# Performance work log

Measured on AMD Instinct MI355X. Metric: run time of the kernel, lower is better.

The kernel has to match this reference:

```python
import jax, jax.numpy as jnp
import numpy as np

N_NODES = 20000
N_EDGES = 8192
UNITS = 128
NUM_GAUSSIANS = 50
CUTOFF = 8.0
GAMMA = 10.0
MIN_DIST, MAX_DIST = 0.0, 30.0


def setup_inputs() -> dict:
    key = jax.random.key(0)
    ks = jax.random.split(key, 6)
    node_features = jax.random.normal(ks[0], (N_NODES, UNITS), dtype=jnp.float32)
    edge_indices = jax.random.randint(ks[1], (2, N_EDGES), 0, N_NODES, dtype=jnp.int32)
    distances = jax.random.uniform(ks[2], (N_EDGES,), dtype=jnp.float32)
    # filter network params (Dense(units) -> swish -> Dense(units*units))
    W1 = jax.random.normal(ks[3], (NUM_GAUSSIANS, UNITS), dtype=jnp.float32) / np.sqrt(NUM_GAUSSIANS)
    b1 = jnp.zeros((UNITS,), dtype=jnp.float32)
    W2 = jax.random.normal(ks[4], (UNITS, UNITS * UNITS), dtype=jnp.float32) / np.sqrt(UNITS)
    b2 = jnp.zeros((UNITS * UNITS,), dtype=jnp.float32)
    # transform Dense(units, use_bias=False)
    Wt = jax.random.normal(ks[5], (UNITS, UNITS), dtype=jnp.float32) / np.sqrt(UNITS)
    return {"node_features": node_features, "edge_indices": edge_indices,
            "distances": distances, "W1": W1, "b1": b1, "W2": W2, "b2": b2, "Wt": Wt}


def reference(node_features, edge_indices, distances, W1, b1, W2, b2, Wt):
    n_nodes, units = node_features.shape
    # cutoff mask (multiplicative; dropped edges contribute zero to the scatter-sum,
    # equivalent to tf.boolean_mask + unsorted_segment_sum)
    mask = (distances <= CUTOFF).astype(node_features.dtype)  # [E]
    # Gaussian basis expansion
    centers = jnp.linspace(MIN_DIST, MAX_DIST, NUM_GAUSSIANS, dtype=jnp.float32)
    df = jnp.exp(-GAMMA * jnp.square(distances[:, None] - centers[None, :]))  # [E, G]
    # filter network: Dense -> swish -> Dense(units*units)
    h = jax.nn.silu(df @ W1 + b1)                    # [E, U]
    filters = (h @ W2 + b2).reshape(-1, units, units)  # [E, U, U]
    # gather source node features, transform, per-edge matvec
    src = node_features[edge_indices[0]]             # [E, U]
    transformed = src @ Wt                           # [E, U]
    filtered = jnp.einsum('eij,ej->ei', filters, transformed) * mask[:, None]  # [E, U]
    # scatter-sum to destination nodes
    messages = jax.ops.segment_sum(filtered, edge_indices[1], num_segments=n_nodes)
    return jax.nn.silu(messages)
```

## Files before the change

### kernel.cpp

```cpp
#include <hip/hip_runtime.h>
#include <hip/hip_fp16.h>


typedef _Float16 f16;
typedef __attribute__((ext_vector_type(8))) f16 f16x8;
typedef __attribute__((ext_vector_type(4))) float f32x4;
typedef __attribute__((ext_vector_type(4))) unsigned int u32x4;

#define NEDGE 8192
#define NNODE 20000
#define NG    50
#define KSTEPS 516
#define W2C_BYTES (KSTEPS * 8192)
#define HT_BYTES (64 * 132 * 128 * 2)
#define TM_BYTES (NEDGE * 128 * 2)
#define WTC_BYTES (4 * 8 * 64 * 8 * 2)
#define W1C_BYTES (2 * 8 * 64 * 8 * 2)
#define FP_BYTES ((size_t)8 * NEDGE * 128 * 4)

#define LDS_H   0
#define LDS_TM  5120
#define LDS_TOT 37888

#define K1_SRC 0
#define K1_DF  16384
#define K1_MSK 24576
#define K1_TOT 24832

static __device__ __forceinline__ float fsilu(float x) { return x / (1.0f + __expf(-x)); }

static __device__ __forceinline__ void gll16(const void* g, void* l) {
  __builtin_amdgcn_global_load_lds(
      (const __attribute__((address_space(1))) unsigned int*)g,
      (__attribute__((address_space(3))) unsigned int*)l, 16, 0, 0);
}

__global__ __launch_bounds__(256) void kprep(const float* __restrict__ W2,
                                             const float* __restrict__ b2,
                                             const float* __restrict__ W1,
                                             const float* __restrict__ B1,
                                             const float* __restrict__ WT,
                                             f16* __restrict__ w2c,
                                             f16* __restrict__ wtc,
                                             f16* __restrict__ w1c,
                                             float* __restrict__ out, int nz4) {
  const int bid = blockIdx.x, tid = threadIdx.x;

  if (bid < 516) {
    const int u = bid >> 2, s = bid & 3;
    const int i = tid >> 1, half = tid & 1;
    const float* src = ((u < 128) ? (W2 + (size_t)u * 16384) : b2)
                       + i * 128 + s * 32 + half * 16;
    union { f16 s16[16]; u32x4 v[2]; } pk;
#pragma unroll
    for (int q = 0; q < 4; ++q) {
      f32x4 v = *(const f32x4*)(src + q * 4);
#pragma unroll
      for (int r = 0; r < 4; ++r) pk.s16[q * 4 + r] = (f16)v[r];
    }
    const int nt = i >> 4, l15 = i & 15;
    u32x4* dst = (u32x4*)w2c + (size_t)(u * 4 + s) * 512 + nt * 64 + l15;
    dst[(half * 2 + 0) * 16] = pk.v[0];
    dst[(half * 2 + 1) * 16] = pk.v[1];
    return;
  }
  if (bid < 520) {
    int step = bid - 516;
#pragma unroll
    for (int q = 0; q < 2; ++q) {
      int fi = q * 256 + tid;
      int lane = fi & 63, nt = fi >> 6;
      int j = nt * 16 + (lane & 15);
      union { f16 s[8]; u32x4 v; } pk;
#pragma unroll
      for (int r = 0; r < 8; ++r) {
        int u = step * 32 + (lane >> 4) * 8 + r;
        pk.s[r] = (f16)WT[u * 128 + j];
      }
      *((u32x4*)wtc + (step * 8 + nt) * 64 + lane) = pk.v;
    }
    return;
  }
  if (bid == 520) {
#pragma unroll
    for (int q = 0; q < 4; ++q) {
      int fi = q * 256 + tid;
      int lane = fi & 63, nt = (fi >> 6) & 7, step = fi >> 9;
      int j = nt * 16 + (lane & 15);
      union { f16 s[8]; u32x4 v; } pk;
#pragma unroll
      for (int r = 0; r < 8; ++r) {
        int g = step * 32 + (lane >> 4) * 8 + r;
        float v = (g < 50) ? W1[g * 128 + j] : ((g == 63) ? B1[j] : 0.0f);
        pk.s[r] = (f16)v;
      }
      *((u32x4*)w1c + (step * 8 + nt) * 64 + lane) = pk.v;
    }
    return;
  }
  {
    int base = (bid - 521) * 1024;
    f32x4 z = {0.f, 0.f, 0.f, 0.f};
#pragma unroll
    for (int k = 0; k < 4; ++k) {
      int i4 = base + k * 256 + tid;
      if (i4 < nz4) ((f32x4*)out)[i4] = z;
    }
  }
}

__global__ __launch_bounds__(256) void k1m(const float* __restrict__ NF,
                                           const int*   __restrict__ EI,
                                           const float* __restrict__ DI,
                                           const f16* __restrict__ wtc,
                                           const f16* __restrict__ w1c,
                                           f16* __restrict__ ht2,
                                           f16* __restrict__ tmo) {
  __shared__ u32x4 smem_v[K1_TOT / 16];
  char* smem = (char*)smem_v;
  const int bid = blockIdx.x, tid = threadIdx.x;
  const int e0g = bid * 64;
  const int eb  = bid >> 1;
  const int el0 = (bid & 1) * 64;

  if (tid < 64) {
    float d = DI[e0g + tid];
    *(float*)(smem + K1_MSK + tid * 4) = (d <= 8.0f) ? 1.0f : 0.0f;
  }
  {
    int e = tid >> 2, g0 = (tid & 3) * 16;
    float d = DI[e0g + e];
    union { f16 s[16]; u32x4 v[2]; } pk;
#pragma unroll
    for (int gg = 0; gg < 16; ++gg) {
      int g = g0 + gg;
      float x = d - (float)g * (30.0f / 49.0f);
      float v = (g < 50) ? __expf(-10.0f * x * x) : ((g == 63) ? 1.0f : 0.0f);
      pk.s[gg] = (f16)v;
    }
    int base = e * 128 + g0 * 2, sw = (e & 7) << 4;
    *(u32x4*)(smem + K1_DF + ((base) ^ sw))      = pk.v[0];
    *(u32x4*)(smem + K1_DF + ((base + 16) ^ sw)) = pk.v[1];
  }
#pragma unroll
  for (int p = 0; p < 8; ++p) {
    int e = p * 8 + (tid >> 5);
    int u0 = (tid & 31) * 4;
    int row = EI[e0g + e];
    f32x4 v = *(const f32x4*)(NF + (size_t)row * 128 + u0);
    union { f16 s[4]; unsigned long long q; } pk;
#pragma unroll
    for (int r = 0; r < 4; ++r) pk.s[r] = (f16)v[r];
    int addr = e * 256 + u0 * 2;
    *(unsigned long long*)(smem + K1_SRC + (addr ^ ((e & 7) << 4))) = pk.q;
  }
  __syncthreads();

  const int w = tid >> 6, lane = tid & 63;
  const int l15 = lane & 15, g4 = lane >> 4;
  const int erow = w * 16;
  const int asw = (l15 & 7) << 4;

  f32x4 at[8], ah[8];
#pragma unroll
  for (int nt = 0; nt < 8; ++nt) {
    at[nt] = (f32x4){0.f, 0.f, 0.f, 0.f};
    ah[nt] = (f32x4){0.f, 0.f, 0.f, 0.f};
  }
  const f16x8* wtp = (const f16x8*)wtc;
  const f16x8* w1p = (const f16x8*)w1c;

#pragma unroll
  for (int step = 0; step < 4; ++step) {
    int aaddr = (erow + l15) * 256 + step * 64 + g4 * 16;
    f16x8 a = *(const f16x8*)(smem + K1_SRC + (aaddr ^ asw));
#pragma unroll
    for (int nt = 0; nt < 8; ++nt)
      at[nt] = __builtin_amdgcn_mfma_f32_16x16x32_f16(a, wtp[(step * 8 + nt) * 64 + lane], at[nt], 0, 0, 0);
  }
#pragma unroll
  for (int step = 0; step < 2; ++step) {
    int aaddr = (erow + l15) * 128 + step * 64 + g4 * 16;
    f16x8 a = *(const f16x8*)(smem + K1_DF + (aaddr ^ asw));
#pragma unroll
    for (int nt = 0; nt < 8; ++nt)
      ah[nt] = __builtin_amdgcn_mfma_f32_16x16x32_f16(a, w1p[(step * 8 + nt) * 64 + lane], ah[nt], 0, 0, 0);
  }

  const float* mk = (const float*)(smem + K1_MSK);
#pragma unroll
  for (int r = 0; r < 4; ++r) {
    int el_ = erow + g4 * 4 + r;
    float m = mk[el_];
    int sw2 = (el_ & 7) << 4;
    char* rowp = (char*)tmo + (size_t)(e0g + el_) * 256;
#pragma unroll
    for (int nt = 0; nt < 8; ++nt)
      *(f16*)(rowp + (((nt * 16 + l15) * 2) ^ sw2)) = (f16)(m * at[nt][r]);
  }
#pragma unroll
  for (int r = 0; r < 4; ++r) {
    int el_ = el0 + erow + g4 * 4 + r;
#pragma unroll
    for (int nt = 0; nt < 8; ++nt) {
      int u = nt * 16 + l15;
      ht2[((size_t)eb * 132 + u) * 128 + el_] = (f16)fsilu(ah[nt][r]);
    }
  }
  if (tid < 64) ht2[((size_t)eb * 132 + 128) * 128 + el0 + tid] = (f16)1.0f;
}

template<int MODE>
__global__ __launch_bounds__(256, 2) void k2_gemm(const f16* __restrict__ w2c,
                                                  const f16* __restrict__ ht2,
                                                  const f16* __restrict__ tm,
                                                  const int* __restrict__ EI,
                                                  float* __restrict__ fpart,
                                                  float* __restrict__ msg) {
  __shared__ u32x4 smem_v[LDS_TOT / 16];
  char* smem = (char*)smem_v;

  const int bid = blockIdx.x;
  const int c   = bid & 7;
  const int eb  = bid >> 3;
  const int e0  = eb * 128;
  const int nu  = (c == 7) ? 17 : 16;
  const int tid = threadIdx.x, w = tid >> 6, lane = tid & 63;
  const int l15 = lane & 15, g4 = lane >> 4;
  const int wm = w >> 1, wn = w & 1;

  const char* bp = (const char*)w2c + (size_t)(c * 64) * 8192 + wn * 4096 + lane * 16;
  f16x8 B0[4], B1[4];
#pragma unroll
  for (int nt = 0; nt < 4; ++nt) B0[nt] = *(const f16x8*)(bp + nt * 1024);
#pragma unroll
  for (int nt = 0; nt < 4; ++nt) B1[nt] = *(const f16x8*)(bp + 8192 + nt * 1024);

  {
    const char* tsrc = (const char*)tm + (size_t)e0 * 256 + w * 8192;
#pragma unroll
    for (int q = 0; q < 8; ++q)
      gll16(tsrc + q * 1024 + lane * 16,
            smem + LDS_TM + w * 8192 + q * 1024 + lane * 16);
  }
  if (w == 0) {
    const char* hsrc = (const char*)ht2 + ((size_t)eb * 132 + c * 16) * 256;
#pragma unroll
    for (int q = 0; q < 5; ++q)
      gll16(hsrc + q * 1024 + lane * 16, smem + LDS_H + q * 1024 + lane * 16);
  }
  __syncthreads();

  f16x8 Tall[4][4];
  {
    const int tmrow = LDS_TM + (wm * 64 + l15) * 256;
    const int colsw = (l15 & 7) << 4;
#pragma unroll
    for (int rt = 0; rt < 4; ++rt)
#pragma unroll
      for (int jc = 0; jc < 4; ++jc)
        Tall[rt][jc] = *(const f16x8*)(smem + tmrow + rt * 4096 +
                                       ((jc * 64 + g4 * 16) ^ colsw));
  }
  const __half* hbase = (const __half*)(smem + LDS_H) + wm * 64 + l15;

  __half2 hc[4], hn[4];
#pragma unroll
  for (int rt = 0; rt < 4; ++rt) hc[rt] = __half2half2(hbase[rt * 16]);

  size_t off = 2 * 8192;
  f32x4 acc[4][4];
#pragma unroll
  for (int rt = 0; rt < 4; ++rt)
#pragma unroll
    for (int nt = 0; nt < 4; ++nt) acc[rt][nt] = (f32x4){0.f, 0.f, 0.f, 0.f};

  for (int u = 0; u < nu; ++u) {
#pragma unroll
    for (int jc = 0; jc < 4; ++jc) {
      if (jc == 1) {
#pragma unroll
        for (int rt = 0; rt < 4; ++rt)
          hn[rt] = __half2half2(hbase[(u + 1) * 128 + rt * 16]);
      }
      union uf { f16x8 v; __half2 h[4]; };
      uf a[4];
#pragma unroll
      for (int rt = 0; rt < 4; ++rt) {
        uf t; t.v = Tall[rt][jc];
#pragma unroll
        for (int q = 0; q < 4; ++q) a[rt].h[q] = __hmul2(t.h[q], hc[rt]);
      }
      __builtin_amdgcn_s_setprio(1);
#pragma unroll
      for (int nt = 0; nt < 4; ++nt) {
        if ((jc & 1) == 0) {
#pragma unroll
          for (int rt = 0; rt < 4; ++rt)
            acc[rt][nt] = __builtin_amdgcn_mfma_f32_16x16x32_f16(a[rt].v, B0[nt], acc[rt][nt], 0, 0, 0);
          B0[nt] = *(const f16x8*)(bp + off + nt * 1024);
        } else {
#pragma unroll
          for (int rt = 0; rt < 4; ++rt)
            acc[rt][nt] = __builtin_amdgcn_mfma_f32_16x16x32_f16(a[rt].v, B1[nt], acc[rt][nt], 0, 0, 0);
          B1[nt] = *(const f16x8*)(bp + off + nt * 1024);
        }
      }
      __builtin_amdgcn_s_setprio(0);
      off += 8192;
    }
#pragma unroll
    for (int rt = 0; rt < 4; ++rt) hc[rt] = hn[rt];
  }

  if (MODE == 0) {
#pragma unroll
    for (int rt = 0; rt < 4; ++rt) {
#pragma unroll
      for (int r = 0; r < 4; ++r) {
        int e = e0 + wm * 64 + rt * 16 + g4 * 4 + r;
        float* prow = fpart + ((size_t)c * NEDGE + e) * 128 + wn * 64 + l15;
#pragma unroll
        for (int nt = 0; nt < 4; ++nt)
          prow[nt * 16] = acc[rt][nt][r];
      }
    }
  } else {
    const int* dst = EI + NEDGE;
#pragma unroll
    for (int rt = 0; rt < 4; ++rt) {
#pragma unroll
      for (int r = 0; r < 4; ++r) {
        int e = e0 + wm * 64 + rt * 16 + g4 * 4 + r;
        float* row = msg + (size_t)dst[e] * 128 + wn * 64 + l15;
#pragma unroll
        for (int nt = 0; nt < 4; ++nt)
          atomicAdd(row + nt * 16, acc[rt][nt][r]);
      }
    }
  }
}

__global__ __launch_bounds__(256) void k4_reduce(const float* __restrict__ fp,
                                                 const int* __restrict__ EI,
                                                 float* __restrict__ out) {
  int gid = blockIdx.x * 256 + threadIdx.x;
  int e  = gid >> 5;
  int i0 = (gid & 31) << 2;
  f32x4 s = {0.f, 0.f, 0.f, 0.f};
#pragma unroll
  for (int cc = 0; cc < 8; ++cc) {
    f32x4 v = *(const f32x4*)(fp + ((size_t)cc * NEDGE + e) * 128 + i0);
    s[0] += v[0]; s[1] += v[1]; s[2] += v[2]; s[3] += v[3];
  }
  float* row = out + (size_t)EI[NEDGE + e] * 128 + i0;
  atomicAdd(row + 0, s[0]);
  atomicAdd(row + 1, s[1]);
  atomicAdd(row + 2, s[2]);
  atomicAdd(row + 3, s[3]);
}

__global__ __launch_bounds__(256) void k3_silu(float* __restrict__ out, int n4) {
  int idx = blockIdx.x * 256 + threadIdx.x;
  int stride = gridDim.x * 256;
  f32x4* p = (f32x4*)out;
  for (; idx < n4; idx += stride) {
    f32x4 v = p[idx];
#pragma unroll
    for (int cc = 0; cc < 4; ++cc) v[cc] = fsilu(v[cc]);
    p[idx] = v;
  }
}

extern "C" void kernel_launch(void* const* d_in, const int* in_sizes, int n_in,
                              void* d_out, int out_size, void* d_ws, size_t ws_size,
                              hipStream_t stream) {
  const float* NF = (const float*)d_in[0];
  const int*   EI = (const int*)  d_in[1];
  const float* DI = (const float*)d_in[2];
  const float* W1 = (const float*)d_in[3];
  const float* B1 = (const float*)d_in[4];
  const float* W2 = (const float*)d_in[5];
  const float* B2 = (const float*)d_in[6];
  const float* WT = (const float*)d_in[7];
  float* out = (float*)d_out;

  char* base = (char*)d_ws;
  f16*   w2c = (f16*)base;
  f16*   ht2 = (f16*)(base + W2C_BYTES);
  f16*   tmo = (f16*)(base + W2C_BYTES + HT_BYTES);
  f16*   wtc = (f16*)(base + W2C_BYTES + HT_BYTES + TM_BYTES);
  f16*   w1c = (f16*)(base + W2C_BYTES + HT_BYTES + TM_BYTES + WTC_BYTES);
  float* fp  = (float*)(base + W2C_BYTES + HT_BYTES + TM_BYTES + WTC_BYTES + W1C_BYTES);
  size_t need_min  = (size_t)W2C_BYTES + HT_BYTES + TM_BYTES + WTC_BYTES + W1C_BYTES;
  size_t need_fast = need_min + FP_BYTES;
  if (ws_size < need_min) return;
  const bool fast = (ws_size >= need_fast);

  int nz4 = out_size / 4;
  kprep<<<dim3(1146), dim3(256), 0, stream>>>(W2, B2, W1, B1, WT, w2c, wtc, w1c, out, nz4);
  k1m  <<<dim3(128),  dim3(256), 0, stream>>>(NF, EI, DI, wtc, w1c, ht2, tmo);
  if (fast) {
    k2_gemm<0><<<dim3(512),  dim3(256), 0, stream>>>(w2c, ht2, tmo, EI, fp, out);
    k4_reduce <<<dim3(1024), dim3(256), 0, stream>>>(fp, EI, out);
  } else {
    k2_gemm<1><<<dim3(512),  dim3(256), 0, stream>>>(w2c, ht2, tmo, EI, fp, out);
  }
  k3_silu<<<dim3(1024), dim3(256), 0, stream>>>(out, nz4);
}
```

Before: 83.83 us.

## Fuse edge-prep kernel into weight-prep launch with per-block LDS weights; reorder partials

Merges the k1m edge kernel into the weight-conversion kernel. Each of the 128 edge blocks now converts Wt and W1 to fp16 itself straight into LDS, so the separate wtc/w1c global buffers and one kernel launch go away. The partial-sum buffer layout changes to edge-major so k4_reduce reads its 8 partials contiguously. The trade is that every block repeats the Wt/W1 conversion and LDS use grows to about 74KB, which lowers occupancy for all blocks of the merged kernel, including the W2-conversion blocks.

```diff
diff --git a/kernel.cpp b/kernel.cpp
--- a/kernel.cpp
+++ b/kernel.cpp
@@ -14,18 +14,18 @@
 #define W2C_BYTES (KSTEPS * 8192)
 #define HT_BYTES (64 * 132 * 128 * 2)
 #define TM_BYTES (NEDGE * 128 * 2)
-#define WTC_BYTES (4 * 8 * 64 * 8 * 2)
-#define W1C_BYTES (2 * 8 * 64 * 8 * 2)
-#define FP_BYTES ((size_t)8 * NEDGE * 128 * 4)
+#define FP_BYTES ((size_t)NEDGE * 8 * 128 * 4)
 
 #define LDS_H   0
 #define LDS_TM  5120
 #define LDS_TOT 37888
 
-#define K1_SRC 0
-#define K1_DF  16384
-#define K1_MSK 24576
-#define K1_TOT 24832
+#define K_SRC 0
+#define K_DF  16384
+#define K_MSK 24576
+#define K_WTC 24832
+#define K_W1C 57600
+#define K_TOT 73984
 
 static __device__ __forceinline__ float fsilu(float x) { return x / (1.0f + __expf(-x)); }
 
@@ -35,15 +35,20 @@
       (__attribute__((address_space(3))) unsigned int*)l, 16, 0, 0);
 }
 
-__global__ __launch_bounds__(256) void kprep(const float* __restrict__ W2,
-                                             const float* __restrict__ b2,
-                                             const float* __restrict__ W1,
-                                             const float* __restrict__ B1,
-                                             const float* __restrict__ WT,
-                                             f16* __restrict__ w2c,
-                                             f16* __restrict__ wtc,
-                                             f16* __restrict__ w1c,
-                                             float* __restrict__ out, int nz4) {
+__global__ __launch_bounds__(256) void kpre(const float* __restrict__ W2,
+                                            const float* __restrict__ b2,
+                                            const float* __restrict__ W1,
+                                            const float* __restrict__ B1,
+                                            const float* __restrict__ WT,
+                                            const float* __restrict__ NF,
+                                            const int*   __restrict__ EI,
+                                            const float* __restrict__ DI,
+                                            f16* __restrict__ w2c,
+                                            f16* __restrict__ ht2,
+                                            f16* __restrict__ tmo,
+                                            float* __restrict__ out, int nz4) {
+  __shared__ u32x4 smem_v[K_TOT / 16];
+  char* smem = (char*)smem_v;
   const int bid = blockIdx.x, tid = threadIdx.x;
 
   if (bid < 516) {
@@ -64,28 +69,27 @@
     dst[(half * 2 + 1) * 16] = pk.v[1];
     return;
   }
-  if (bid < 520) {
-    int step = bid - 516;
-#pragma unroll
-    for (int q = 0; q < 2; ++q) {
-      int fi = q * 256 + tid;
-      int lane = fi & 63, nt = fi >> 6;
+  if (bid < 644) {
+    const int bid2 = bid - 516;
+    const int e0g = bid2 * 64;
+    const int eb  = bid2 >> 1;
+    const int el0 = (bid2 & 1) * 64;
+
+#pragma unroll
+    for (int q = 0; q < 8; ++q) {
+      int f = q * 256 + tid;
+      int lane = f & 63, nt = (f >> 6) & 7, step = f >> 9;
       int j = nt * 16 + (lane & 15);
+      int u0 = step * 32 + (lane >> 4) * 8;
       union { f16 s[8]; u32x4 v; } pk;
 #pragma unroll
-      for (int r = 0; r < 8; ++r) {
-        int u = step * 32 + (lane >> 4) * 8 + r;
-        pk.s[r] = (f16)WT[u * 128 + j];
-      }
-      *((u32x4*)wtc + (step * 8 + nt) * 64 + lane) = pk.v;
-    }
-    return;
-  }
-  if (bid == 520) {
+      for (int r = 0; r < 8; ++r) pk.s[r] = (f16)WT[(u0 + r) * 128 + j];
+      *(u32x4*)(smem + K_WTC + f * 16) = pk.v;
+    }
 #pragma unroll
     for (int q = 0; q < 4; ++q) {
-      int fi = q * 256 + tid;
-      int lane = fi & 63, nt = (fi >> 6) & 7, step = fi >> 9;
+      int f = q * 256 + tid;
+      int lane = f & 63, nt = (f >> 6) & 7, step = f >> 9;
       int j = nt * 16 + (lane & 15);
       union { f16 s[8]; u32x4 v; } pk;
 #pragma unroll
@@ -94,12 +98,97 @@
         float v = (g < 50) ? W1[g * 128 + j] : ((g == 63) ? B1[j] : 0.0f);
         pk.s[r] = (f16)v;
       }
-      *((u32x4*)w1c + (step * 8 + nt) * 64 + lane) = pk.v;
-    }
+      *(u32x4*)(smem + K_W1C + f * 16) = pk.v;
+    }
+    if (tid < 64) {
+      float d = DI[e0g + tid];
+      *(float*)(smem + K_MSK + tid * 4) = (d <= 8.0f) ? 1.0f : 0.0f;
+    }
+    {
+      int e = tid >> 2, g0 = (tid & 3) * 16;
+      float d = DI[e0g + e];
+      union { f16 s[16]; u32x4 v[2]; } pk;
+#pragma unroll
+      for (int gg = 0; gg < 16; ++gg) {
+        int g = g0 + gg;
+        float x = d - (float)g * (30.0f / 49.0f);
+        float v = (g < 50) ? __expf(-10.0f * x * x) : ((g == 63) ? 1.0f : 0.0f);
+        pk.s[gg] = (f16)v;
+      }
+      int base = e * 128 + g0 * 2, sw = (e & 7) << 4;
+      *(u32x4*)(smem + K_DF + ((base) ^ sw))      = pk.v[0];
+      *(u32x4*)(smem + K_DF + ((base + 16) ^ sw)) = pk.v[1];
+    }
+#pragma unroll
+    for (int p = 0; p < 8; ++p) {
+      int e = p * 8 + (tid >> 5);
+      int u0 = (tid & 31) * 4;
+      int row = EI[e0g + e];
+      f32x4 v = *(const f32x4*)(NF + (size_t)row * 128 + u0);
+      union { f16 s[4]; unsigned long long q; } pk;
+#pragma unroll
+      for (int r = 0; r < 4; ++r) pk.s[r] = (f16)v[r];
+      int addr = e * 256 + u0 * 2;
+      *(unsigned long long*)(smem + K_SRC + (addr ^ ((e & 7) << 4))) = pk.q;
+    }
+    __syncthreads();
+
+    const int w = tid >> 6, lane = tid & 63;
+    const int l15 = lane & 15, g4 = lane >> 4;
+    const int erow = w * 16;
+    const int asw = (l15 & 7) << 4;
+
+    f32x4 at[8], ah[8];
+#pragma unroll
+    for (int nt = 0; nt < 8; ++nt) {
+      at[nt] = (f32x4){0.f, 0.f, 0.f, 0.f};
+      ah[nt] = (f32x4){0.f, 0.f, 0.f, 0.f};
+    }
+#pragma unroll
+    for (int step = 0; step < 4; ++step) {
+      int aaddr = (erow + l15) * 256 + step * 64 + g4 * 16;
+      f16x8 a = *(const f16x8*)(smem + K_SRC + (aaddr ^ asw));
+#pragma unroll
+      for (int nt = 0; nt < 8; ++nt) {
+        f16x8 b = *(const f16x8*)(smem + K_WTC + ((step * 8 + nt) * 64 + lane) * 16);
+        at[nt] = __builtin_amdgcn_mfma_f32_16x16x32_f16(a, b, at[nt], 0, 0, 0);
+      }
+    }
+#pragma unroll
+    for (int step = 0; step < 2; ++step) {
+      int aaddr = (erow + l15) * 128 + step * 64 + g4 * 16;
+      f16x8 a = *(const f16x8*)(smem + K_DF + (aaddr ^ asw));
+#pragma unroll
+      for (int nt = 0; nt < 8; ++nt) {
+        f16x8 b = *(const f16x8*)(smem + K_W1C + ((step * 8 + nt) * 64 + lane) * 16);
+        ah[nt] = __builtin_amdgcn_mfma_f32_16x16x32_f16(a, b, ah[nt], 0, 0, 0);
+      }
+    }
+    const float* mk = (const float*)(smem + K_MSK);
+#pragma unroll
+    for (int r = 0; r < 4; ++r) {
+      int el_ = erow + g4 * 4 + r;
+      float m = mk[el_];
+      int sw2 = (el_ & 7) << 4;
+      char* rowp = (char*)tmo + (size_t)(e0g + el_) * 256;
+#pragma unroll
+      for (int nt = 0; nt < 8; ++nt)
+        *(f16*)(rowp + (((nt * 16 + l15) * 2) ^ sw2)) = (f16)(m * at[nt][r]);
+    }
+#pragma unroll
+    for (int r = 0; r < 4; ++r) {
+      int el_ = el0 + erow + g4 * 4 + r;
+#pragma unroll
+      for (int nt = 0; nt < 8; ++nt) {
+        int u = nt * 16 + l15;
+        ht2[((size_t)eb * 132 + u) * 128 + el_] = (f16)fsilu(ah[nt][r]);
+      }
+    }
+    if (tid < 64) ht2[((size_t)eb * 132 + 128) * 128 + el0 + tid] = (f16)1.0f;
     return;
   }
   {
-    int base = (bid - 521) * 1024;
+    int base = (bid - 644) * 1024;
     f32x4 z = {0.f, 0.f, 0.f, 0.f};
 #pragma unroll
     for (int k = 0; k < 4; ++k) {
@@ -107,107 +196,6 @@
       if (i4 < nz4) ((f32x4*)out)[i4] = z;
     }
   }
-}
-
-__global__ __launch_bounds__(256) void k1m(const float* __restrict__ NF,
-                                           const int*   __restrict__ EI,
-                                           const float* __restrict__ DI,
-                                           const f16* __restrict__ wtc,
-                                           const f16* __restrict__ w1c,
-                                           f16* __restrict__ ht2,
-                                           f16* __restrict__ tmo) {
-  __shared__ u32x4 smem_v[K1_TOT / 16];
-  char* smem = (char*)smem_v;
-  const int bid = blockIdx.x, tid = threadIdx.x;
-  const int e0g = bid * 64;
-  const int eb  = bid >> 1;
-  const int el0 = (bid & 1) * 64;
-
-  if (tid < 64) {
-    float d = DI[e0g + tid];
-    *(float*)(smem + K1_MSK + tid * 4) = (d <= 8.0f) ? 1.0f : 0.0f;
-  }
-  {
-    int e = tid >> 2, g0 = (tid & 3) * 16;
-    float d = DI[e0g + e];
-    union { f16 s[16]; u32x4 v[2]; } pk;
-#pragma unroll
-    for (int gg = 0; gg < 16; ++gg) {
-      int g = g0 + gg;
-      float x = d - (float)g * (30.0f / 49.0f);
-      float v = (g < 50) ? __expf(-10.0f * x * x) : ((g == 63) ? 1.0f : 0.0f);
-      pk.s[gg] = (f16)v;
-    }
-    int base = e * 128 + g0 * 2, sw = (e & 7) << 4;
-    *(u32x4*)(smem + K1_DF + ((base) ^ sw))      = pk.v[0];
-    *(u32x4*)(smem + K1_DF + ((base + 16) ^ sw)) = pk.v[1];
-  }
-#pragma unroll
-  for (int p = 0; p < 8; ++p) {
-    int e = p * 8 + (tid >> 5);
-    int u0 = (tid & 31) * 4;
-    int row = EI[e0g + e];
-    f32x4 v = *(const f32x4*)(NF + (size_t)row * 128 + u0);
-    union { f16 s[4]; unsigned long long q; } pk;
-#pragma unroll
-    for (int r = 0; r < 4; ++r) pk.s[r] = (f16)v[r];
-    int addr = e * 256 + u0 * 2;
-    *(unsigned long long*)(smem + K1_SRC + (addr ^ ((e & 7) << 4))) = pk.q;
-  }
-  __syncthreads();
-
-  const int w = tid >> 6, lane = tid & 63;
-  const int l15 = lane & 15, g4 = lane >> 4;
-  const int erow = w * 16;
-  const int asw = (l15 & 7) << 4;
-
-  f32x4 at[8], ah[8];
-#pragma unroll
-  for (int nt = 0; nt < 8; ++nt) {
-    at[nt] = (f32x4){0.f, 0.f, 0.f, 0.f};
-    ah[nt] = (f32x4){0.f, 0.f, 0.f, 0.f};
-  }
-  const f16x8* wtp = (const f16x8*)wtc;
-  const f16x8* w1p = (const f16x8*)w1c;
-
-#pragma unroll
-  for (int step = 0; step < 4; ++step) {
-    int aaddr = (erow + l15) * 256 + step * 64 + g4 * 16;
-    f16x8 a = *(const f16x8*)(smem + K1_SRC + (aaddr ^ asw));
-#pragma unroll
-    for (int nt = 0; nt < 8; ++nt)
-      at[nt] = __builtin_amdgcn_mfma_f32_16x16x32_f16(a, wtp[(step * 8 + nt) * 64 + lane], at[nt], 0, 0, 0);
-  }
-#pragma unroll
-  for (int step = 0; step < 2; ++step) {
-    int aaddr = (erow + l15) * 128 + step * 64 + g4 * 16;
-    f16x8 a = *(const f16x8*)(smem + K1_DF + (aaddr ^ asw));
-#pragma unroll
-    for (int nt = 0; nt < 8; ++nt)
-      ah[nt] = __builtin_amdgcn_mfma_f32_16x16x32_f16(a, w1p[(step * 8 + nt) * 64 + lane], ah[nt], 0, 0, 0);
-  }
-
-  const float* mk = (const float*)(smem + K1_MSK);
-#pragma unroll
-  for (int r = 0; r < 4; ++r) {
-    int el_ = erow + g4 * 4 + r;
-    float m = mk[el_];
-    int sw2 = (el_ & 7) << 4;
-    char* rowp = (char*)tmo + (size_t)(e0g + el_) * 256;
-#pragma unroll
-    for (int nt = 0; nt < 8; ++nt)
-      *(f16*)(rowp + (((nt * 16 + l15) * 2) ^ sw2)) = (f16)(m * at[nt][r]);
-  }
-#pragma unroll
-  for (int r = 0; r < 4; ++r) {
-    int el_ = el0 + erow + g4 * 4 + r;
-#pragma unroll
-    for (int nt = 0; nt < 8; ++nt) {
-      int u = nt * 16 + l15;
-      ht2[((size_t)eb * 132 + u) * 128 + el_] = (f16)fsilu(ah[nt][r]);
-    }
-  }
-  if (tid < 64) ht2[((size_t)eb * 132 + 128) * 128 + el0 + tid] = (f16)1.0f;
 }
 
 template<int MODE>
@@ -319,7 +307,7 @@
 #pragma unroll
       for (int r = 0; r < 4; ++r) {
         int e = e0 + wm * 64 + rt * 16 + g4 * 4 + r;
-        float* prow = fpart + ((size_t)c * NEDGE + e) * 128 + wn * 64 + l15;
+        float* prow = fpart + ((size_t)e * 8 + c) * 128 + wn * 64 + l15;
 #pragma unroll
         for (int nt = 0; nt < 4; ++nt)
           prow[nt * 16] = acc[rt][nt][r];
@@ -347,10 +335,11 @@
   int gid = blockIdx.x * 256 + threadIdx.x;
   int e  = gid >> 5;
   int i0 = (gid & 31) << 2;
+  const float* ep = fp + (size_t)e * 1024 + i0;
   f32x4 s = {0.f, 0.f, 0.f, 0.f};
 #pragma unroll
   for (int cc = 0; cc < 8; ++cc) {
-    f32x4 v = *(const f32x4*)(fp + ((size_t)cc * NEDGE + e) * 128 + i0);
+    f32x4 v = *(const f32x4*)(ep + cc * 128);
     s[0] += v[0]; s[1] += v[1]; s[2] += v[2]; s[3] += v[3];
   }
   float* row = out + (size_t)EI[NEDGE + e] * 128 + i0;
@@ -389,17 +378,16 @@
   f16*   w2c = (f16*)base;
   f16*   ht2 = (f16*)(base + W2C_BYTES);
   f16*   tmo = (f16*)(base + W2C_BYTES + HT_BYTES);
-  f16*   wtc = (f16*)(base + W2C_BYTES + HT_BYTES + TM_BYTES);
-  f16*   w1c = (f16*)(base + W2C_BYTES + HT_BYTES + TM_BYTES + WTC_BYTES);
-  float* fp  = (float*)(base + W2C_BYTES + HT_BYTES + TM_BYTES + WTC_BYTES + W1C_BYTES);
-  size_t need_min  = (size_t)W2C_BYTES + HT_BYTES + TM_BYTES + WTC_BYTES + W1C_BYTES;
+  float* fp  = (float*)(base + W2C_BYTES + HT_BYTES + TM_BYTES);
+  size_t need_min  = (size_t)W2C_BYTES + HT_BYTES + TM_BYTES;
   size_t need_fast = need_min + FP_BYTES;
   if (ws_size < need_min) return;
   const bool fast = (ws_size >= need_fast);
 
   int nz4 = out_size / 4;
-  kprep<<<dim3(1146), dim3(256), 0, stream>>>(W2, B2, W1, B1, WT, w2c, wtc, w1c, out, nz4);
-  k1m  <<<dim3(128),  dim3(256), 0, stream>>>(NF, EI, DI, wtc, w1c, ht2, tmo);
+  int zb  = (nz4 + 1023) / 1024;
+  kpre<<<dim3(644 + zb), dim3(256), 0, stream>>>(W2, B2, W1, B1, WT, NF, EI, DI,
+                                                 w2c, ht2, tmo, out, nz4);
   if (fast) {
     k2_gemm<0><<<dim3(512),  dim3(256), 0, stream>>>(w2c, ht2, tmo, EI, fp, out);
     k4_reduce <<<dim3(1024), dim3(256), 0, stream>>>(fp, EI, out);
```

Measured after the change: 82.20 us, median of 2. No clear change (-1.9%).
